# Performance work log

Hardware: AMD Instinct MI355X
Metric: run time of the kernel (lower is better)

## Reference

```python
import jax, jax.numpy as jnp
import numpy as np

N = 100000   # nodes
E = 1600000  # edges
D = 128      # input_dim
H = 128      # hidden_dim
O = 64       # output_dim


def setup_inputs() -> dict:
    key = jax.random.key(0)
    ks = jax.random.split(key, 8)
    x = jax.random.normal(ks[0], (N, D), dtype=jnp.float32)
    edge_index = jax.random.randint(ks[1], (2, E), 0, N, dtype=jnp.int32)
    # Glorot-ish init for weights, zeros for biases (matches GCNConv/Linear defaults in spirit)
    W1 = jax.random.normal(ks[2], (D, H), dtype=jnp.float32) / np.sqrt(D)
    b1 = jnp.zeros((H,), dtype=jnp.float32)
    W2 = jax.random.normal(ks[3], (H, H), dtype=jnp.float32) / np.sqrt(H)
    b2 = jnp.zeros((H,), dtype=jnp.float32)
    Wf = jax.random.normal(ks[4], (H, O), dtype=jnp.float32) / np.sqrt(H)
    bf = jnp.zeros((O,), dtype=jnp.float32)
    return {"x": x, "W1": W1, "b1": b1, "W2": W2, "b2": b2,
            "Wf": Wf, "bf": bf, "edge_index": edge_index}


def gcn_conv(x, W, b, src, dst):
    """GCNConv: out = D^{-1/2} (A + I) D^{-1/2} (x W) + b, edges given as (src->dst)."""
    n = x.shape[0]
    h = x @ W  # [N, H]
    loop = jnp.arange(n, dtype=src.dtype)
    s = jnp.concatenate([src, loop])  # add self-loops
    d = jnp.concatenate([dst, loop])
    deg = jax.ops.segment_sum(jnp.ones_like(s, dtype=h.dtype), d, num_segments=n)
    dinv = jnp.where(deg > 0, jax.lax.rsqrt(deg), 0.0)
    coef = dinv[s] * dinv[d]                              # [E+N]
    msg = h[s] * coef[:, None]                            # gather + scale
    out = jax.ops.segment_sum(msg, d, num_segments=n)     # scatter-add aggregate
    return out + b


def reference(x, W1, b1, W2, b2, Wf, bf, edge_index):
    src, dst = edge_index[0], edge_index[1]
    h = jax.nn.relu(gcn_conv(x, W1, b1, src, dst))
    # dropout is identity in eval mode
    h = jax.nn.relu(gcn_conv(h, W2, b2, src, dst))
    return h @ Wf + bf
```

## Files before the change

### kernel.cpp

```cpp
#include <hip/hip_runtime.h>

#define FD 128
#define SCAN_B 256
#define SCAN_T 256


__global__ void k_deg(const int* __restrict__ dst, int* __restrict__ deg, int E) {
  int e = blockIdx.x * blockDim.x + threadIdx.x;
  if (e < E) atomicAdd(&deg[dst[e]], 1);
}


__global__ __launch_bounds__(SCAN_T) void k_part(const int* __restrict__ deg,
                                                 float* __restrict__ dinv,
                                                 int* __restrict__ part, int n) {
  const int b = blockIdx.x;
  const int chunk = (n + SCAN_B - 1) / SCAN_B;
  const int lo = b * chunk;
  const int hi = min(lo + chunk, n);
  int sum = 0;
  for (int i = lo + threadIdx.x; i < hi; i += SCAN_T) {
    int d = deg[i];
    sum += d;
    dinv[i] = rsqrtf((float)(d + 1));
  }
  __shared__ int red[SCAN_T / 64];
  for (int off = 32; off > 0; off >>= 1) sum += __shfl_down(sum, off, 64);
  if ((threadIdx.x & 63) == 0) red[threadIdx.x >> 6] = sum;
  __syncthreads();
  if (threadIdx.x == 0) {
    int s = 0;
#pragma unroll
    for (int w = 0; w < SCAN_T / 64; ++w) s += red[w];
    part[b] = s;
  }
}

__global__ __launch_bounds__(SCAN_B) void k_scanpart(int* __restrict__ part,
                                                     int* __restrict__ row_ptr, int n) {
  __shared__ int s[SCAN_B];
  const int t = threadIdx.x;
  int v = part[t];
  s[t] = v;
  __syncthreads();
  for (int off = 1; off < SCAN_B; off <<= 1) {
    int u = (t >= off) ? s[t - off] : 0;
    __syncthreads();
    s[t] += u;
    __syncthreads();
  }
  part[t] = s[t] - v;
  if (t == SCAN_B - 1) row_ptr[n] = s[t];
}

__global__ __launch_bounds__(SCAN_T) void k_rowptr(const int* __restrict__ deg,
                                                   const int* __restrict__ part,
                                                   int* __restrict__ row_ptr,
                                                   int* __restrict__ cursor, int n) {
  const int b = blockIdx.x;
  const int chunk = (n + SCAN_B - 1) / SCAN_B;
  const int lo = b * chunk;
  const int hi = min(lo + chunk, n);
  const int sub = (chunk + SCAN_T - 1) / SCAN_T;
  const int t = threadIdx.x;
  const int slo = min(lo + t * sub, hi);
  const int shi = min(slo + sub, hi);
  int sum = 0;
  for (int i = slo; i < shi; ++i) sum += deg[i];
  __shared__ int s[SCAN_T];
  s[t] = sum;
  __syncthreads();
  for (int off = 1; off < SCAN_T; off <<= 1) {
    int u = (t >= off) ? s[t - off] : 0;
    __syncthreads();
    s[t] += u;
    __syncthreads();
  }
  int run = part[b] + s[t] - sum;
  for (int i = slo; i < shi; ++i) {
    row_ptr[i] = run;
    cursor[i]  = run;
    run += deg[i];
  }
}


__global__ void k_fill(const int* __restrict__ src, const int* __restrict__ dst,
                       const float* __restrict__ dinv, int* __restrict__ cursor,
                       int* __restrict__ csr_src, float* __restrict__ csr_coef, int E) {
  int e = blockIdx.x * blockDim.x + threadIdx.x;
  if (e < E) {
    int s = src[e], d = dst[e];
    int pos = atomicAdd(&cursor[d], 1);
    csr_src[pos]  = s;
    csr_coef[pos] = dinv[s] * dinv[d];
  }
}


__global__ __launch_bounds__(256) void k_gemm(const float* __restrict__ A,
                                              const float* __restrict__ W, int ldw,
                                              const float* __restrict__ bias,
                                              float* __restrict__ out, int ldo, int nrows) {
  __shared__ float Ws[64 * 64];
  __shared__ float xs[64][129];
  const int t  = threadIdx.x;
  const int c0 = blockIdx.y * 64;
  const int r0 = blockIdx.x * 64;

  for (int i = t; i < 64 * 32; i += 256) {
    int r  = i >> 5;
    int k4 = (i & 31) << 2;
    int row = r0 + r;
    float4 v = make_float4(0.f, 0.f, 0.f, 0.f);
    if (row < nrows) v = *reinterpret_cast<const float4*>(&A[(size_t)row * FD + k4]);
    xs[r][k4 + 0] = v.x; xs[r][k4 + 1] = v.y; xs[r][k4 + 2] = v.z; xs[r][k4 + 3] = v.w;
  }

  const int r  = t & 31;
  const int cb = (t >> 5) << 3;
  float acc0[8], acc1[8];
#pragma unroll
  for (int j = 0; j < 8; ++j) {
    float bz = bias ? bias[c0 + cb + j] : 0.f;
    acc0[j] = bz; acc1[j] = bz;
  }

  for (int half = 0; half < 2; ++half) {
    __syncthreads();
    for (int i = t; i < 64 * 16; i += 256) {
      int k  = i >> 4;
      int c4 = (i & 15) << 2;
      *reinterpret_cast<float4*>(&Ws[k * 64 + c4]) =
          *reinterpret_cast<const float4*>(&W[(size_t)(half * 64 + k) * ldw + c0 + c4]);
    }
    __syncthreads();
    const int kbase = half * 64;
#pragma unroll 8
    for (int k = 0; k < 64; ++k) {
      float x0 = xs[r][kbase + k];
      float x1 = xs[r + 32][kbase + k];
      const float4 w0 = *reinterpret_cast<const float4*>(&Ws[k * 64 + cb]);
      const float4 w1 = *reinterpret_cast<const float4*>(&Ws[k * 64 + cb + 4]);
      acc0[0] += x0 * w0.x; acc0[1] += x0 * w0.y; acc0[2] += x0 * w0.z; acc0[3] += x0 * w0.w;
      acc0[4] += x0 * w1.x; acc0[5] += x0 * w1.y; acc0[6] += x0 * w1.z; acc0[7] += x0 * w1.w;
      acc1[0] += x1 * w0.x; acc1[1] += x1 * w0.y; acc1[2] += x1 * w0.z; acc1[3] += x1 * w0.w;
      acc1[4] += x1 * w1.x; acc1[5] += x1 * w1.y; acc1[6] += x1 * w1.z; acc1[7] += x1 * w1.w;
    }
  }

  const int row0 = r0 + r, row1 = r0 + r + 32;
  if (row0 < nrows) {
    float* o = &out[(size_t)row0 * ldo + c0 + cb];
    *reinterpret_cast<float4*>(o)     = make_float4(acc0[0], acc0[1], acc0[2], acc0[3]);
    *reinterpret_cast<float4*>(o + 4) = make_float4(acc0[4], acc0[5], acc0[6], acc0[7]);
  }
  if (row1 < nrows) {
    float* o = &out[(size_t)row1 * ldo + c0 + cb];
    *reinterpret_cast<float4*>(o)     = make_float4(acc1[0], acc1[1], acc1[2], acc1[3]);
    *reinterpret_cast<float4*>(o + 4) = make_float4(acc1[4], acc1[5], acc1[6], acc1[7]);
  }
}


__global__ __launch_bounds__(256) void k_agg(const float* __restrict__ h,
                                             const int* __restrict__ row_ptr,
                                             const int* __restrict__ csr_src,
                                             const float* __restrict__ csr_coef,
                                             const float* __restrict__ dinv,
                                             const float* __restrict__ bias,
                                             float* __restrict__ out, int n) {
  const int node = blockIdx.x * 4 + (threadIdx.x >> 6);
  if (node >= n) return;
  const int f2 = (threadIdx.x & 63) << 1;
  const float di = dinv[node];
  float2 hv = *reinterpret_cast<const float2*>(&h[(size_t)node * FD + f2]);
  float accx = hv.x * di * di;
  float accy = hv.y * di * di;
  const int e0 = row_ptr[node], e1 = row_ptr[node + 1];
  int e = e0;
  for (; e + 2 <= e1; e += 2) {
    int s0   = csr_src[e];
    int s1   = csr_src[e + 1];
    float c0 = csr_coef[e];
    float c1 = csr_coef[e + 1];
    float2 v0 = *reinterpret_cast<const float2*>(&h[(size_t)s0 * FD + f2]);
    float2 v1 = *reinterpret_cast<const float2*>(&h[(size_t)s1 * FD + f2]);
    accx += v0.x * c0; accy += v0.y * c0;
    accx += v1.x * c1; accy += v1.y * c1;
  }
  if (e < e1) {
    int s   = csr_src[e];
    float c = csr_coef[e];
    float2 v = *reinterpret_cast<const float2*>(&h[(size_t)s * FD + f2]);
    accx += v.x * c; accy += v.y * c;
  }
  float2 o;
  o.x = fmaxf(accx + bias[f2],     0.f);
  o.y = fmaxf(accy + bias[f2 + 1], 0.f);
  *reinterpret_cast<float2*>(&out[(size_t)node * FD + f2]) = o;
}


extern "C" void kernel_launch(void* const* d_in, const int* in_sizes, int n_in,
                              void* d_out, int out_size, void* d_ws, size_t ws_size,
                              hipStream_t stream) {
  const float* x  = (const float*)d_in[0];
  const float* W1 = (const float*)d_in[1];
  const float* b1 = (const float*)d_in[2];
  const float* W2 = (const float*)d_in[3];
  const float* b2 = (const float*)d_in[4];
  const float* Wf = (const float*)d_in[5];
  const float* bf = (const float*)d_in[6];
  const int*   ei = (const int*)d_in[7];

  const int N = in_sizes[0] / FD;
  const int E = in_sizes[7] / 2;
  const int O = in_sizes[6];
  const int* src = ei;
  const int* dst = ei + E;

  char* ws = (char*)d_ws;
  size_t off = 0;
  auto alloc = [&](size_t bytes) -> void* {
    void* p = ws + off;
    off += (bytes + 255) & ~(size_t)255;
    return p;
  };
  float* A        = (float*)alloc((size_t)N * FD * 4);
  float* B        = (float*)alloc((size_t)N * FD * 4);
  int*   deg      = (int*)  alloc((size_t)N * 4);
  float* dinv     = (float*)alloc((size_t)N * 4);
  int*   row_ptr  = (int*)  alloc((size_t)(N + 1) * 4);
  int*   cursor   = (int*)  alloc((size_t)N * 4);
  int*   csr_src  = (int*)  alloc((size_t)E * 4);
  float* csr_coef = (float*)alloc((size_t)E * 4);
  int*   part     = (int*)  alloc((size_t)SCAN_B * 4);

  hipMemsetAsync(deg, 0, (size_t)N * 4, stream);
  k_deg     <<<(E + 255) / 256, 256, 0, stream>>>(dst, deg, E);
  k_part    <<<SCAN_B, SCAN_T, 0, stream>>>(deg, dinv, part, N);
  k_scanpart<<<1, SCAN_B, 0, stream>>>(part, row_ptr, N);
  k_rowptr  <<<SCAN_B, SCAN_T, 0, stream>>>(deg, part, row_ptr, cursor, N);
  k_fill    <<<(E + 255) / 256, 256, 0, stream>>>(src, dst, dinv, cursor, csr_src, csr_coef, E);

  const int gx = (N + 63) / 64;
  k_gemm<<<dim3(gx, 2), 256, 0, stream>>>(x, W1, FD, nullptr, A, FD, N);
  k_agg <<<(N + 3) / 4, 256, 0, stream>>>(A, row_ptr, csr_src, csr_coef, dinv, b1, B, N);
  k_gemm<<<dim3(gx, 2), 256, 0, stream>>>(B, W2, FD, nullptr, A, FD, N);
  k_agg <<<(N + 3) / 4, 256, 0, stream>>>(A, row_ptr, csr_src, csr_coef, dinv, b2, B, N);
  k_gemm<<<dim3(gx, 1), 256, 0, stream>>>(B, Wf, O, bf, (float*)d_out, O, N);
}
```

Before: 694.5 us.

## Interleave CSR src/coef, unroll aggregation by four, enlarge GEMM register tile

Packs each CSR entry's source index and coefficient into one int2 so the aggregation loop does one 8-byte load per edge instead of two separate streams. The aggregation loop is unrolled from two to four neighbors so more independent gathers are in flight. The GEMM now handles 128 rows per block with a 4x8 register tile per thread, reading A transposed from LDS with float4 loads. This should raise arithmetic intensity and cut LDS traffic per FMA, at the cost of more registers and a strided LDS write pattern during the transpose.

```diff
diff --git a/kernel.cpp b/kernel.cpp
--- a/kernel.cpp
+++ b/kernel.cpp
@@ -87,86 +87,93 @@
 
 __global__ void k_fill(const int* __restrict__ src, const int* __restrict__ dst,
                        const float* __restrict__ dinv, int* __restrict__ cursor,
-                       int* __restrict__ csr_src, float* __restrict__ csr_coef, int E) {
+                       int2* __restrict__ csr, int E) {
   int e = blockIdx.x * blockDim.x + threadIdx.x;
   if (e < E) {
     int s = src[e], d = dst[e];
     int pos = atomicAdd(&cursor[d], 1);
-    csr_src[pos]  = s;
-    csr_coef[pos] = dinv[s] * dinv[d];
-  }
-}
-
-
-__global__ __launch_bounds__(256) void k_gemm(const float* __restrict__ A,
+    csr[pos] = make_int2(s, __float_as_int(dinv[s] * dinv[d]));
+  }
+}
+
+
+__global__ __launch_bounds__(256) void k_gemm(const float* __restrict__ A, int lda,
                                               const float* __restrict__ W, int ldw,
                                               const float* __restrict__ bias,
                                               float* __restrict__ out, int ldo, int nrows) {
   __shared__ float Ws[64 * 64];
-  __shared__ float xs[64][129];
+  __shared__ float xsT[64 * 128];
   const int t  = threadIdx.x;
   const int c0 = blockIdx.y * 64;
-  const int r0 = blockIdx.x * 64;
-
-  for (int i = t; i < 64 * 32; i += 256) {
-    int r  = i >> 5;
-    int k4 = (i & 31) << 2;
-    int row = r0 + r;
-    float4 v = make_float4(0.f, 0.f, 0.f, 0.f);
-    if (row < nrows) v = *reinterpret_cast<const float4*>(&A[(size_t)row * FD + k4]);
-    xs[r][k4 + 0] = v.x; xs[r][k4 + 1] = v.y; xs[r][k4 + 2] = v.z; xs[r][k4 + 3] = v.w;
-  }
-
-  const int r  = t & 31;
-  const int cb = (t >> 5) << 3;
-  float acc0[8], acc1[8];
-#pragma unroll
-  for (int j = 0; j < 8; ++j) {
-    float bz = bias ? bias[c0 + cb + j] : 0.f;
-    acc0[j] = bz; acc1[j] = bz;
-  }
+  const int r0 = blockIdx.x * 128;
+
+  const int rgrp = t & 31;
+  const int cgrp = t >> 5;
+
+  float acc[4][8];
+#pragma unroll
+  for (int i = 0; i < 4; ++i)
+#pragma unroll
+    for (int j = 0; j < 8; ++j)
+      acc[i][j] = bias ? bias[c0 + cgrp * 8 + j] : 0.f;
+
+  const int rr = t & 127;
+  const int hk = t >> 7;
 
   for (int half = 0; half < 2; ++half) {
+    const int kbase = half * 64;
     __syncthreads();
     for (int i = t; i < 64 * 16; i += 256) {
       int k  = i >> 4;
       int c4 = (i & 15) << 2;
       *reinterpret_cast<float4*>(&Ws[k * 64 + c4]) =
-          *reinterpret_cast<const float4*>(&W[(size_t)(half * 64 + k) * ldw + c0 + c4]);
-    }
-    __syncthreads();
-    const int kbase = half * 64;
-#pragma unroll 8
+          *reinterpret_cast<const float4*>(&W[(size_t)(kbase + k) * ldw + c0 + c4]);
+    }
+    {
+      const int row = r0 + rr;
+      const float* ap = &A[(size_t)row * lda + kbase + hk * 32];
+#pragma unroll
+      for (int j = 0; j < 8; ++j) {
+        float4 v = make_float4(0.f, 0.f, 0.f, 0.f);
+        if (row < nrows) v = *reinterpret_cast<const float4*>(ap + j * 4);
+        const int kb = hk * 32 + j * 4;
+        xsT[(kb + 0) * 128 + rr] = v.x;
+        xsT[(kb + 1) * 128 + rr] = v.y;
+        xsT[(kb + 2) * 128 + rr] = v.z;
+        xsT[(kb + 3) * 128 + rr] = v.w;
+      }
+    }
+    __syncthreads();
+#pragma unroll 4
     for (int k = 0; k < 64; ++k) {
-      float x0 = xs[r][kbase + k];
-      float x1 = xs[r + 32][kbase + k];
-      const float4 w0 = *reinterpret_cast<const float4*>(&Ws[k * 64 + cb]);
-      const float4 w1 = *reinterpret_cast<const float4*>(&Ws[k * 64 + cb + 4]);
-      acc0[0] += x0 * w0.x; acc0[1] += x0 * w0.y; acc0[2] += x0 * w0.z; acc0[3] += x0 * w0.w;
-      acc0[4] += x0 * w1.x; acc0[5] += x0 * w1.y; acc0[6] += x0 * w1.z; acc0[7] += x0 * w1.w;
-      acc1[0] += x1 * w0.x; acc1[1] += x1 * w0.y; acc1[2] += x1 * w0.z; acc1[3] += x1 * w0.w;
-      acc1[4] += x1 * w1.x; acc1[5] += x1 * w1.y; acc1[6] += x1 * w1.z; acc1[7] += x1 * w1.w;
-    }
-  }
-
-  const int row0 = r0 + r, row1 = r0 + r + 32;
-  if (row0 < nrows) {
-    float* o = &out[(size_t)row0 * ldo + c0 + cb];
-    *reinterpret_cast<float4*>(o)     = make_float4(acc0[0], acc0[1], acc0[2], acc0[3]);
-    *reinterpret_cast<float4*>(o + 4) = make_float4(acc0[4], acc0[5], acc0[6], acc0[7]);
-  }
-  if (row1 < nrows) {
-    float* o = &out[(size_t)row1 * ldo + c0 + cb];
-    *reinterpret_cast<float4*>(o)     = make_float4(acc1[0], acc1[1], acc1[2], acc1[3]);
-    *reinterpret_cast<float4*>(o + 4) = make_float4(acc1[4], acc1[5], acc1[6], acc1[7]);
+      const float4 xv = *reinterpret_cast<const float4*>(&xsT[k * 128 + rgrp * 4]);
+      const float4 w0 = *reinterpret_cast<const float4*>(&Ws[k * 64 + cgrp * 8]);
+      const float4 w1 = *reinterpret_cast<const float4*>(&Ws[k * 64 + cgrp * 8 + 4]);
+      const float x[4] = {xv.x, xv.y, xv.z, xv.w};
+      const float w[8] = {w0.x, w0.y, w0.z, w0.w, w1.x, w1.y, w1.z, w1.w};
+#pragma unroll
+      for (int i = 0; i < 4; ++i)
+#pragma unroll
+        for (int j = 0; j < 8; ++j)
+          acc[i][j] += x[i] * w[j];
+    }
+  }
+
+#pragma unroll
+  for (int i = 0; i < 4; ++i) {
+    const int row = r0 + rgrp * 4 + i;
+    if (row < nrows) {
+      float* o = &out[(size_t)row * ldo + c0 + cgrp * 8];
+      *reinterpret_cast<float4*>(o)     = make_float4(acc[i][0], acc[i][1], acc[i][2], acc[i][3]);
+      *reinterpret_cast<float4*>(o + 4) = make_float4(acc[i][4], acc[i][5], acc[i][6], acc[i][7]);
+    }
   }
 }
 
 
 __global__ __launch_bounds__(256) void k_agg(const float* __restrict__ h,
                                              const int* __restrict__ row_ptr,
-                                             const int* __restrict__ csr_src,
-                                             const float* __restrict__ csr_coef,
+                                             const int2* __restrict__ csr,
                                              const float* __restrict__ dinv,
                                              const float* __restrict__ bias,
                                              float* __restrict__ out, int n) {
@@ -179,20 +186,28 @@
   float accy = hv.y * di * di;
   const int e0 = row_ptr[node], e1 = row_ptr[node + 1];
   int e = e0;
-  for (; e + 2 <= e1; e += 2) {
-    int s0   = csr_src[e];
-    int s1   = csr_src[e + 1];
-    float c0 = csr_coef[e];
-    float c1 = csr_coef[e + 1];
-    float2 v0 = *reinterpret_cast<const float2*>(&h[(size_t)s0 * FD + f2]);
-    float2 v1 = *reinterpret_cast<const float2*>(&h[(size_t)s1 * FD + f2]);
+  for (; e + 4 <= e1; e += 4) {
+    const int2 E0 = csr[e];
+    const int2 E1 = csr[e + 1];
+    const int2 E2 = csr[e + 2];
+    const int2 E3 = csr[e + 3];
+    const float2 v0 = *reinterpret_cast<const float2*>(&h[(size_t)E0.x * FD + f2]);
+    const float2 v1 = *reinterpret_cast<const float2*>(&h[(size_t)E1.x * FD + f2]);
+    const float2 v2 = *reinterpret_cast<const float2*>(&h[(size_t)E2.x * FD + f2]);
+    const float2 v3 = *reinterpret_cast<const float2*>(&h[(size_t)E3.x * FD + f2]);
+    const float c0 = __int_as_float(E0.y);
+    const float c1 = __int_as_float(E1.y);
+    const float c2 = __int_as_float(E2.y);
+    const float c3 = __int_as_float(E3.y);
     accx += v0.x * c0; accy += v0.y * c0;
     accx += v1.x * c1; accy += v1.y * c1;
-  }
-  if (e < e1) {
-    int s   = csr_src[e];
-    float c = csr_coef[e];
-    float2 v = *reinterpret_cast<const float2*>(&h[(size_t)s * FD + f2]);
+    accx += v2.x * c2; accy += v2.y * c2;
+    accx += v3.x * c3; accy += v3.y * c3;
+  }
+  for (; e < e1; ++e) {
+    const int2 E0 = csr[e];
+    const float c = __int_as_float(E0.y);
+    const float2 v = *reinterpret_cast<const float2*>(&h[(size_t)E0.x * FD + f2]);
     accx += v.x * c; accy += v.y * c;
   }
   float2 o;
@@ -227,27 +242,26 @@
     off += (bytes + 255) & ~(size_t)255;
     return p;
   };
-  float* A        = (float*)alloc((size_t)N * FD * 4);
-  float* B        = (float*)alloc((size_t)N * FD * 4);
-  int*   deg      = (int*)  alloc((size_t)N * 4);
-  float* dinv     = (float*)alloc((size_t)N * 4);
-  int*   row_ptr  = (int*)  alloc((size_t)(N + 1) * 4);
-  int*   cursor   = (int*)  alloc((size_t)N * 4);
-  int*   csr_src  = (int*)  alloc((size_t)E * 4);
-  float* csr_coef = (float*)alloc((size_t)E * 4);
-  int*   part     = (int*)  alloc((size_t)SCAN_B * 4);
+  float* A       = (float*)alloc((size_t)N * FD * 4);
+  float* B       = (float*)alloc((size_t)N * FD * 4);
+  int*   deg     = (int*)  alloc((size_t)N * 4);
+  float* dinv    = (float*)alloc((size_t)N * 4);
+  int*   row_ptr = (int*)  alloc((size_t)(N + 1) * 4);
+  int*   cursor  = (int*)  alloc((size_t)N * 4);
+  int2*  csr     = (int2*) alloc((size_t)E * 8);
+  int*   part    = (int*)  alloc((size_t)SCAN_B * 4);
 
   hipMemsetAsync(deg, 0, (size_t)N * 4, stream);
   k_deg     <<<(E + 255) / 256, 256, 0, stream>>>(dst, deg, E);
   k_part    <<<SCAN_B, SCAN_T, 0, stream>>>(deg, dinv, part, N);
   k_scanpart<<<1, SCAN_B, 0, stream>>>(part, row_ptr, N);
   k_rowptr  <<<SCAN_B, SCAN_T, 0, stream>>>(deg, part, row_ptr, cursor, N);
-  k_fill    <<<(E + 255) / 256, 256, 0, stream>>>(src, dst, dinv, cursor, csr_src, csr_coef, E);
-
-  const int gx = (N + 63) / 64;
-  k_gemm<<<dim3(gx, 2), 256, 0, stream>>>(x, W1, FD, nullptr, A, FD, N);
-  k_agg <<<(N + 3) / 4, 256, 0, stream>>>(A, row_ptr, csr_src, csr_coef, dinv, b1, B, N);
-  k_gemm<<<dim3(gx, 2), 256, 0, stream>>>(B, W2, FD, nullptr, A, FD, N);
-  k_agg <<<(N + 3) / 4, 256, 0, stream>>>(A, row_ptr, csr_src, csr_coef, dinv, b2, B, N);
-  k_gemm<<<dim3(gx, 1), 256, 0, stream>>>(B, Wf, O, bf, (float*)d_out, O, N);
-}
+  k_fill    <<<(E + 255) / 256, 256, 0, stream>>>(src, dst, dinv, cursor, csr, E);
+
+  const int gx = (N + 127) / 128;
+  k_gemm<<<dim3(gx, 2), 256, 0, stream>>>(x, FD, W1, FD, nullptr, A, FD, N);
+  k_agg <<<(N + 3) / 4, 256, 0, stream>>>(A, row_ptr, csr, dinv, b1, B, N);
+  k_gemm<<<dim3(gx, 2), 256, 0, stream>>>(B, FD, W2, FD, nullptr, A, FD, N);
+  k_agg <<<(N + 3) / 4, 256, 0, stream>>>(A, row_ptr, csr, dinv, b2, B, N);
+  k_gemm<<<dim3(gx, 1), 256, 0, stream>>>(B, FD, Wf, O, bf, (float*)d_out, O, N);
+}
```

After: 643.3 us. 7.4% less time.
